# Kernel tuning notes

Hardware: AMD Instinct MI355X
Metric: run time of the kernel (lower is better)

## Reference

```python
import jax, jax.numpy as jnp
import numpy as np

B, SQ, SD, H = 64, 64, 512, 128


def setup_inputs() -> dict:
    key = jax.random.key(0)
    k1, k2, k3, k4, k5 = jax.random.split(key, 5)
    q = jax.random.normal(k1, (B, SQ, H), dtype=jnp.float32)
    d_pos = jax.random.normal(k2, (B, SD, H), dtype=jnp.float32)
    d_neg = jax.random.normal(k3, (B, SD, H), dtype=jnp.float32)
    mask_pos = jax.random.randint(k4, (B, SD), 0, 2, dtype=jnp.int32).at[:, 0].set(1)
    mask_neg = jax.random.randint(k5, (B, SD), 0, 2, dtype=jnp.int32).at[:, 0].set(1)
    return {"q": q, "d_pos": d_pos, "d_neg": d_neg,
            "mask_pos": mask_pos, "mask_neg": mask_neg}


def _colbert_maxsim(q, d, mask):
    # q: [a, s, h], d: [b, t, h], mask: [b, t] -> scores [a, b]
    simis = jnp.einsum('ash,bth->abst', q, d)            # [a, b, s, t]
    simis = jnp.where(mask[None, :, None, :] == 0, -jnp.inf, simis)
    return simis.max(axis=3).sum(axis=2)                 # max over t, sum over s


def reference(q, d_pos, d_neg, mask_pos, mask_neg):
    # Concatenate pos and in-batch-negative score blocks -> [B, 2B]
    distances = jnp.concatenate(
        [_colbert_maxsim(q, d_pos, mask_pos),
         _colbert_maxsim(q, d_neg, mask_neg)], axis=1)
    labels = jnp.arange(q.shape[0])
    logp = jax.nn.log_softmax(distances, axis=1)
    loss = -jnp.take_along_axis(logp, labels[:, None], axis=1).mean()
    return loss
```

## Files before the change

kernel.cpp:

```cpp
#include <hip/hip_runtime.h>
#include <hip/hip_bf16.h>
#include <math.h>
#include <stdint.h>

#define BB 64
#define SQN 64
#define SDN 512
#define HH 128

typedef __attribute__((ext_vector_type(8))) short bf16x8;
typedef __attribute__((ext_vector_type(16))) float f32x16;

__device__ __forceinline__ short f2bf(float f) {
  union { float f; unsigned u; } x; x.f = f;
  unsigned r = x.u + 0x7fffu + ((x.u >> 16) & 1u);
  return (short)(r >> 16);
}

__device__ __forceinline__ void gl_lds16(const short* g, short* l) {
  __builtin_amdgcn_global_load_lds(
      (const __attribute__((address_space(1))) unsigned int*)g,
      (__attribute__((address_space(3))) unsigned int*)l, 16, 0, 0);
}

__global__ __launch_bounds__(256)
void convert_kernel(const float* __restrict__ q, const float* __restrict__ dp,
                    const float* __restrict__ dn,
                    const int* __restrict__ mp, const int* __restrict__ mn,
                    short* __restrict__ oq, short* __restrict__ od,
                    int* __restrict__ nchunks, int* __restrict__ counter) {
  const int tid = threadIdx.x;
  if (blockIdx.x < 2048) {
    const int gid = blockIdx.x;
    const int bs  = gid >> 4;
    const int sub = gid & 15;
    const int side = bs >> 6, b = bs & 63;
    const int* mask = side ? mn : mp;
    const float* srcmat = side ? dn : dp;
    __shared__ int perm_lds[SDN];
    __shared__ int pad_s;
    if (tid < 64) {
      int run = 0;
      #pragma unroll
      for (int it = 0; it < SDN / 64; ++it) {
        int t = it * 64 + tid;
        int m = mask[b * SDN + t];
        unsigned long long bal = __ballot(m != 0);
        int pos = run + __popcll(bal & ((1ull << tid) - 1ull));
        if (m) perm_lds[pos] = t;
        run += (int)__popcll(bal);
      }
      int pad = (run + 63) & ~63;
      for (int j = run + tid; j < pad; j += 64) perm_lds[j] = -1;
      if (tid == 0) {
        pad_s = pad;
        if (sub == 0) nchunks[bs] = pad >> 6;
      }
    }
    __syncthreads();
    const int pad = pad_s;
    const int l32 = tid & 31;
    #pragma unroll
    for (int p = 0; p < 4; ++p) {
      int j = sub * 32 + p * 8 + (tid >> 5);
      if (j < pad) {
        int src_t = perm_lds[j];
        float4 v = make_float4(0.f, 0.f, 0.f, 0.f);
        if (src_t >= 0)
          v = ((const float4*)(srcmat + ((size_t)b * SDN + src_t) * HH))[l32];
        short4 o; o.x = f2bf(v.x); o.y = f2bf(v.y); o.z = f2bf(v.z); o.w = f2bf(v.w);
        *(short4*)&od[((size_t)bs * SDN + j) * HH + l32 * 4] = o;
      }
    }
  } else {
    if (blockIdx.x == 2048 && tid == 0) counter[0] = 0;
    const int bq = blockIdx.x - 2048;
    #pragma unroll
    for (int it = 0; it < 16; ++it) {
      int i = bq * 4096 + it * 256 + tid;
      float4 v = ((const float4*)q)[i];
      short4 o; o.x = f2bf(v.x); o.y = f2bf(v.y); o.z = f2bf(v.z); o.w = f2bf(v.w);
      *(short4*)&oq[i * 4] = o;
    }
  }
}

__global__ __launch_bounds__(256, 3)
void maxsim_kernel(const short* __restrict__ qb,
                   const short* __restrict__ dc,
                   const int* __restrict__ nchunks,
                   float* __restrict__ scores,
                   int* __restrict__ counter,
                   float* __restrict__ out) {
  const int aslc = blockIdx.x;
  const int bs0  = blockIdx.y * 4;

  __shared__ __align__(16) short d_lds[2][64 * 128];
  __shared__ int islast_s;

  const int tid = threadIdx.x;
  const int ln  = tid & 63;
  const int w   = tid >> 6;
  const int l31 = ln & 31;
  const int kh  = ln >> 5;
  const int a   = aslc * 4 + w;

  int nchv[4];
  #pragma unroll
  for (int i = 0; i < 4; ++i) nchv[i] = nchunks[bs0 + i];

  bf16x8 qfrag[2][8];
  #pragma unroll
  for (int half = 0; half < 2; ++half) {
    const short* qrow = qb + ((size_t)a * SQN + half * 32 + l31) * HH + kh * 8;
    #pragma unroll
    for (int kc = 0; kc < 8; ++kc)
      qfrag[half][kc] = *(const bf16x8*)(qrow + kc * 16);
  }

  float rmaxh[2] = {0.f, 0.f};

  {
    const short* dsrc = dc + (size_t)bs0 * SDN * HH;
    #pragma unroll
    for (int it = 0; it < 4; ++it) {
      int f = it * 256 + tid;
      int row = f >> 4;
      int c = (f & 15) ^ (row & 15);
      gl_lds16(&dsrc[row * HH + c * 8], &d_lds[0][(it * 256 + w * 64) * 8]);
    }
  }
  __syncthreads();

  int bi = 0, tc = 0, buf = 0;
  for (;;) {
    int nbi = bi, ntc = tc + 1;
    if (ntc == nchv[bi]) { ntc = 0; nbi = bi + 1; }
    const bool hn = (nbi < 4);

    if (hn) {
      const short* dsrc = dc + ((size_t)(bs0 + nbi) * SDN + ntc * 64) * HH;
      short* dst = &d_lds[buf ^ 1][0];
      #pragma unroll
      for (int it = 0; it < 4; ++it) {
        int f = it * 256 + tid;
        int row = f >> 4;
        int c = (f & 15) ^ (row & 15);
        gl_lds16(&dsrc[row * HH + c * 8], &dst[(it * 256 + w * 64) * 8]);
      }
    }

    const short* bufp = &d_lds[buf][0];
    #pragma unroll
    for (int tt = 0; tt < 2; ++tt) {
      int trow = tt * 32 + l31;
      int tm = trow & 15;
      const short* bbase = &bufp[trow * HH];
      f32x16 acc0 = {0,0,0,0,0,0,0,0,0,0,0,0,0,0,0,0};
      f32x16 acc1 = {0,0,0,0,0,0,0,0,0,0,0,0,0,0,0,0};
      #pragma unroll
      for (int kc = 0; kc < 8; ++kc) {
        int c = (kc * 2 + kh) ^ tm;
        bf16x8 dfrag = *(const bf16x8*)&bbase[c * 8];
        acc0 = __builtin_amdgcn_mfma_f32_32x32x16_bf16(dfrag, qfrag[0][kc], acc0, 0, 0, 0);
        acc1 = __builtin_amdgcn_mfma_f32_32x32x16_bf16(dfrag, qfrag[1][kc], acc1, 0, 0, 0);
      }
      float m0 = acc0[0], m1 = acc1[0];
      #pragma unroll
      for (int r = 1; r < 16; ++r) {
        m0 = fmaxf(m0, acc0[r]);
        m1 = fmaxf(m1, acc1[r]);
      }
      rmaxh[0] = fmaxf(rmaxh[0], m0);
      rmaxh[1] = fmaxf(rmaxh[1], m1);
    }

    if (ntc == 0) {
      float v0 = fmaxf(rmaxh[0], __shfl_xor(rmaxh[0], 32));
      float v1 = fmaxf(rmaxh[1], __shfl_xor(rmaxh[1], 32));
      float s = v0 + v1;
      s += __shfl_xor(s, 1);  s += __shfl_xor(s, 2);  s += __shfl_xor(s, 4);
      s += __shfl_xor(s, 8);  s += __shfl_xor(s, 16);
      if (ln == 0) scores[(size_t)a * (2 * BB) + bs0 + bi] = s;
      rmaxh[0] = 0.f; rmaxh[1] = 0.f;
    }

    __syncthreads();
    if (!hn) break;
    bi = nbi; tc = ntc; buf ^= 1;
  }

  __syncthreads();
  if (tid == 0) {
    __threadfence();
    int old = atomicAdd(counter, 1);
    islast_s = (old == 511);
  }
  __syncthreads();
  if (!islast_s) return;
  __threadfence();

  __shared__ float part[4];
  float acc = 0.f;
  for (int i = 0; i < 16; ++i) {
    int r = w * 16 + i;
    float v0 = scores[r * 128 + ln];
    float v1 = scores[r * 128 + 64 + ln];
    float mx = fmaxf(v0, v1);
    #pragma unroll
    for (int off = 32; off >= 1; off >>= 1) mx = fmaxf(mx, __shfl_xor(mx, off));
    float e = __expf(v0 - mx) + __expf(v1 - mx);
    #pragma unroll
    for (int off = 32; off >= 1; off >>= 1) e += __shfl_xor(e, off);
    float lse = mx + __logf(e);
    float diag = __shfl(v0, r);
    acc += lse - diag;
  }
  if (ln == 0) part[w] = acc;
  __syncthreads();
  if (tid == 0)
    out[0] = (part[0] + part[1] + part[2] + part[3]) * (1.0f / 64.0f);
}

extern "C" void kernel_launch(void* const* d_in, const int* in_sizes, int n_in,
                              void* d_out, int out_size, void* d_ws, size_t ws_size,
                              hipStream_t stream) {
  const float* q        = (const float*)d_in[0];
  const float* d_pos    = (const float*)d_in[1];
  const float* d_neg    = (const float*)d_in[2];
  const int*   mask_pos = (const int*)d_in[3];
  const int*   mask_neg = (const int*)d_in[4];

  short* q_bf = (short*)d_ws;
  short* d_c  = q_bf + (size_t)BB * SQN * HH;
  int*   nchunks = (int*)(d_c + (size_t)2 * BB * SDN * HH);
  float* scores  = (float*)(nchunks + 128);
  int*   counter = (int*)(scores + BB * 2 * BB);

  convert_kernel<<<2080, 256, 0, stream>>>(q, d_pos, d_neg, mask_pos, mask_neg,
                                           q_bf, d_c, nchunks, counter);

  dim3 grid(16 , 32 );
  maxsim_kernel<<<grid, 256, 0, stream>>>(q_bf, d_c, nchunks, scores,
                                          counter, (float*)d_out);
}
```

Before: 144.6 us.

## Load document strips directly into registers instead of via shared LDS double-buffer

The maxsim kernel no longer stages 64-row document chunks in LDS through global_load_lds and block-wide barriers. Each wave now loads its own 32-row strip straight from global memory into MFMA fragment registers, double-buffered in two register arrays, and the __syncthreads per chunk is gone. The aim is to remove barrier stalls and LDS traffic. In exchange, the four waves of a block each fetch the same document data from global/L2 (4x the global read traffic), register pressure rises, and the occupancy hint drops from 3 to 2 blocks per CU.

After: 177.9 us. 23.0% more time.

```diff
diff --git a/kernel.cpp b/kernel.cpp
--- a/kernel.cpp
+++ b/kernel.cpp
@@ -15,12 +15,6 @@
   union { float f; unsigned u; } x; x.f = f;
   unsigned r = x.u + 0x7fffu + ((x.u >> 16) & 1u);
   return (short)(r >> 16);
-}
-
-__device__ __forceinline__ void gl_lds16(const short* g, short* l) {
-  __builtin_amdgcn_global_load_lds(
-      (const __attribute__((address_space(1))) unsigned int*)g,
-      (__attribute__((address_space(3))) unsigned int*)l, 16, 0, 0);
 }
 
 __global__ __launch_bounds__(256)
@@ -85,7 +79,7 @@
   }
 }
 
-__global__ __launch_bounds__(256, 3)
+__global__ __launch_bounds__(256, 2)
 void maxsim_kernel(const short* __restrict__ qb,
                    const short* __restrict__ dc,
                    const int* __restrict__ nchunks,
@@ -95,7 +89,6 @@
   const int aslc = blockIdx.x;
   const int bs0  = blockIdx.y * 4;
 
-  __shared__ __align__(16) short d_lds[2][64 * 128];
   __shared__ int islast_s;
 
   const int tid = threadIdx.x;
@@ -105,9 +98,9 @@
   const int kh  = ln >> 5;
   const int a   = aslc * 4 + w;
 
-  int nchv[4];
+  int nstr[4];
   #pragma unroll
-  for (int i = 0; i < 4; ++i) nchv[i] = nchunks[bs0 + i];
+  for (int i = 0; i < 4; ++i) nstr[i] = nchunks[bs0 + i] * 2;
 
   bf16x8 qfrag[2][8];
   #pragma unroll
@@ -120,75 +113,69 @@
 
   float rmaxh[2] = {0.f, 0.f};
 
-  {
-    const short* dsrc = dc + (size_t)bs0 * SDN * HH;
-    #pragma unroll
-    for (int it = 0; it < 4; ++it) {
-      int f = it * 256 + tid;
-      int row = f >> 4;
-      int c = (f & 15) ^ (row & 15);
-      gl_lds16(&dsrc[row * HH + c * 8], &d_lds[0][(it * 256 + w * 64) * 8]);
-    }
-  }
-  __syncthreads();
-
-  int bi = 0, tc = 0, buf = 0;
+#define LOAD_STRIP(dst, bsi, stri) do {                                        \
+    const short* p_ = dc + ((size_t)(bsi) * SDN + (stri) * 32 + l31) * HH + kh * 8; \
+    _Pragma("unroll")                                                          \
+    for (int kc_ = 0; kc_ < 8; ++kc_)                                          \
+      dst[kc_] = *(const bf16x8*)(p_ + kc_ * 16);                              \
+  } while (0)
+
+#define COMPUTE(dv) do {                                                       \
+    f32x16 acc0 = {0,0,0,0,0,0,0,0,0,0,0,0,0,0,0,0};                           \
+    f32x16 acc1 = {0,0,0,0,0,0,0,0,0,0,0,0,0,0,0,0};                           \
+    _Pragma("unroll")                                                          \
+    for (int kc_ = 0; kc_ < 8; ++kc_) {                                        \
+      acc0 = __builtin_amdgcn_mfma_f32_32x32x16_bf16(dv[kc_], qfrag[0][kc_], acc0, 0, 0, 0); \
+      acc1 = __builtin_amdgcn_mfma_f32_32x32x16_bf16(dv[kc_], qfrag[1][kc_], acc1, 0, 0, 0); \
+    }                                                                          \
+    float m0_ = acc0[0], m1_ = acc1[0];                                        \
+    _Pragma("unroll")                                                          \
+    for (int r_ = 1; r_ < 16; ++r_) {                                          \
+      m0_ = fmaxf(m0_, acc0[r_]); m1_ = fmaxf(m1_, acc1[r_]);                  \
+    }                                                                          \
+    rmaxh[0] = fmaxf(rmaxh[0], m0_); rmaxh[1] = fmaxf(rmaxh[1], m1_);          \
+  } while (0)
+
+#define FINALIZE(bii) do {                                                     \
+    float v0_ = fmaxf(rmaxh[0], __shfl_xor(rmaxh[0], 32));                     \
+    float v1_ = fmaxf(rmaxh[1], __shfl_xor(rmaxh[1], 32));                     \
+    float s_ = v0_ + v1_;                                                      \
+    s_ += __shfl_xor(s_, 1);  s_ += __shfl_xor(s_, 2);  s_ += __shfl_xor(s_, 4); \
+    s_ += __shfl_xor(s_, 8);  s_ += __shfl_xor(s_, 16);                        \
+    if (ln == 0) scores[(size_t)a * (2 * BB) + bs0 + (bii)] = s_;              \
+    rmaxh[0] = 0.f; rmaxh[1] = 0.f;                                            \
+  } while (0)
+
+  bf16x8 dA[8], dB[8];
+  int bi = 0, st = 0;
+  LOAD_STRIP(dA, bs0, 0);
+
   for (;;) {
-    int nbi = bi, ntc = tc + 1;
-    if (ntc == nchv[bi]) { ntc = 0; nbi = bi + 1; }
-    const bool hn = (nbi < 4);
-
-    if (hn) {
-      const short* dsrc = dc + ((size_t)(bs0 + nbi) * SDN + ntc * 64) * HH;
-      short* dst = &d_lds[buf ^ 1][0];
-      #pragma unroll
-      for (int it = 0; it < 4; ++it) {
-        int f = it * 256 + tid;
-        int row = f >> 4;
-        int c = (f & 15) ^ (row & 15);
-        gl_lds16(&dsrc[row * HH + c * 8], &dst[(it * 256 + w * 64) * 8]);
-      }
-    }
-
-    const short* bufp = &d_lds[buf][0];
-    #pragma unroll
-    for (int tt = 0; tt < 2; ++tt) {
-      int trow = tt * 32 + l31;
-      int tm = trow & 15;
-      const short* bbase = &bufp[trow * HH];
-      f32x16 acc0 = {0,0,0,0,0,0,0,0,0,0,0,0,0,0,0,0};
-      f32x16 acc1 = {0,0,0,0,0,0,0,0,0,0,0,0,0,0,0,0};
-      #pragma unroll
-      for (int kc = 0; kc < 8; ++kc) {
-        int c = (kc * 2 + kh) ^ tm;
-        bf16x8 dfrag = *(const bf16x8*)&bbase[c * 8];
-        acc0 = __builtin_amdgcn_mfma_f32_32x32x16_bf16(dfrag, qfrag[0][kc], acc0, 0, 0, 0);
-        acc1 = __builtin_amdgcn_mfma_f32_32x32x16_bf16(dfrag, qfrag[1][kc], acc1, 0, 0, 0);
-      }
-      float m0 = acc0[0], m1 = acc1[0];
-      #pragma unroll
-      for (int r = 1; r < 16; ++r) {
-        m0 = fmaxf(m0, acc0[r]);
-        m1 = fmaxf(m1, acc1[r]);
-      }
-      rmaxh[0] = fmaxf(rmaxh[0], m0);
-      rmaxh[1] = fmaxf(rmaxh[1], m1);
-    }
-
-    if (ntc == 0) {
-      float v0 = fmaxf(rmaxh[0], __shfl_xor(rmaxh[0], 32));
-      float v1 = fmaxf(rmaxh[1], __shfl_xor(rmaxh[1], 32));
-      float s = v0 + v1;
-      s += __shfl_xor(s, 1);  s += __shfl_xor(s, 2);  s += __shfl_xor(s, 4);
-      s += __shfl_xor(s, 8);  s += __shfl_xor(s, 16);
-      if (ln == 0) scores[(size_t)a * (2 * BB) + bs0 + bi] = s;
-      rmaxh[0] = 0.f; rmaxh[1] = 0.f;
-    }
-
-    __syncthreads();
-    if (!hn) break;
-    bi = nbi; tc = ntc; buf ^= 1;
-  }
+    {
+      int nbi = bi, nst = st + 1;
+      if (nst == nstr[bi]) { nst = 0; nbi = bi + 1; }
+      const bool hn = (nbi < 4);
+      if (hn) LOAD_STRIP(dB, bs0 + nbi, nst);
+      COMPUTE(dA);
+      if (nst == 0) FINALIZE(bi);
+      if (!hn) break;
+      bi = nbi; st = nst;
+    }
+    {
+      int nbi = bi, nst = st + 1;
+      if (nst == nstr[bi]) { nst = 0; nbi = bi + 1; }
+      const bool hn = (nbi < 4);
+      if (hn) LOAD_STRIP(dA, bs0 + nbi, nst);
+      COMPUTE(dB);
+      if (nst == 0) FINALIZE(bi);
+      if (!hn) break;
+      bi = nbi; st = nst;
+    }
+  }
+
+#undef LOAD_STRIP
+#undef COMPUTE
+#undef FINALIZE
 
   __syncthreads();
   if (tid == 0) {
```
